# Optimization experiments

Measured on AMD Instinct MI355X. Metric: run time of the kernel, lower is better.

The kernel has to match this reference:

```python
import jax, jax.numpy as jnp
import numpy as np

B, S, D, H = 4, 1024, 768, 12
Dh = D // H
EPS = 1e-5


def _layer_norm(x, g, b):
    mu = jnp.mean(x, axis=-1, keepdims=True)
    var = jnp.var(x, axis=-1, keepdims=True)
    return (x - mu) * jax.lax.rsqrt(var + EPS) * g + b


def _mha(q_in, k_in, v_in, Wq, Wk, Wv, Wo, bias):
    # Wq/Wk/Wv: [H, D, Dh] (per-head projections, batched over heads)
    q = jnp.einsum('bsd,hdk->bhsk', q_in, Wq)
    k = jnp.einsum('btd,hdk->bhtk', k_in, Wk)
    v = jnp.einsum('btd,hdk->bhtk', v_in, Wv)
    w = jnp.einsum('bhsk,bhtk->bhst', q, k) * (Dh ** -0.5)
    a = jax.nn.softmax(w + bias, axis=-1)  # bias: 0 / -inf additive mask
    o = jnp.einsum('bhst,bhtk->bhsk', a, v)
    o = o.transpose(0, 2, 1, 3).reshape(q_in.shape[0], q_in.shape[1], H * Dh)  # concat heads
    return o @ Wo


def setup_inputs():
    key = jax.random.key(0)
    ks = jax.random.split(key, 16)
    s = 0.02
    inp = {
        'key_enc': jax.random.normal(ks[0], (B, S, D), jnp.float32),
        'value_enc': jax.random.normal(ks[1], (B, S, D), jnp.float32),
        'x': jax.random.normal(ks[2], (B, S, D), jnp.float32),
        'src_mask': jnp.ones((B, S), jnp.int32),
        'tgt_mask': jnp.ones((B, S), jnp.int32),
        'Wq_m': jax.random.normal(ks[3], (H, D, Dh), jnp.float32) * s,
        'Wk_m': jax.random.normal(ks[4], (H, D, Dh), jnp.float32) * s,
        'Wv_m': jax.random.normal(ks[5], (H, D, Dh), jnp.float32) * s,
        'Wo_m': jax.random.normal(ks[6], (D, D), jnp.float32) * s,
        'Wq_c': jax.random.normal(ks[7], (H, D, Dh), jnp.float32) * s,
        'Wk_c': jax.random.normal(ks[8], (H, D, Dh), jnp.float32) * s,
        'Wv_c': jax.random.normal(ks[9], (H, D, Dh), jnp.float32) * s,
        'Wo_c': jax.random.normal(ks[10], (D, D), jnp.float32) * s,
        'ln1_g': jnp.ones((D,), jnp.float32), 'ln1_b': jnp.zeros((D,), jnp.float32),
        'ln2_g': jnp.ones((D,), jnp.float32), 'ln2_b': jnp.zeros((D,), jnp.float32),
        'ln3_g': jnp.ones((D,), jnp.float32), 'ln3_b': jnp.zeros((D,), jnp.float32),
        'W1': jax.random.normal(ks[11], (D, 4 * D), jnp.float32) * s,
        'b1': jnp.zeros((4 * D,), jnp.float32),
        'W2': jax.random.normal(ks[12], (4 * D, D), jnp.float32) * s,
        'b2': jnp.zeros((D,), jnp.float32),
    }
    return inp


def reference(key_enc, value_enc, x, src_mask, tgt_mask,
              Wq_m, Wk_m, Wv_m, Wo_m, Wq_c, Wk_c, Wv_c, Wo_c,
              ln1_g, ln1_b, ln2_g, ln2_b, ln3_g, ln3_b, W1, b1, W2, b2):
    neg_inf = jnp.float32(-jnp.inf)
    causal = jnp.tril(jnp.ones((S, S), bool))
    # masked self-attn: causal AND target padding mask (mask broadcasts over query rows)
    allow_m = causal[None, None, :, :] & (tgt_mask[:, None, None, :] != 0)
    bias_m = jnp.where(allow_m, jnp.float32(0.0), neg_inf)
    h = _layer_norm(x + _mha(x, x, x, Wq_m, Wk_m, Wv_m, Wo_m, bias_m), ln1_g, ln1_b)
    # cross-attn: keys from `key_enc`, values from `value_enc`, queries from decoder stream
    allow_c = (src_mask[:, None, None, :] != 0)
    bias_c = jnp.where(allow_c, jnp.float32(0.0), neg_inf)
    h = _layer_norm(h + _mha(h, key_enc, value_enc, Wq_c, Wk_c, Wv_c, Wo_c, bias_c), ln2_g, ln2_b)
    # MLP with exact (erf) GELU, as torch nn.GELU default
    mlp = jax.nn.gelu(h @ W1 + b1, approximate=False) @ W2 + b2
    return _layer_norm(h + mlp, ln3_g, ln3_b)
```

## Files before the change

kernel.cpp:

```cpp
#include <hip/hip_runtime.h>
#include <math.h>

#define BB 4
#define SS 1024
#define DD 768
#define HH 12
#define DHD 64
#define MROWS 4096
#define FF 3072
#define WPC (DD * DD)

typedef unsigned short u16;
typedef float f32x4 __attribute__((ext_vector_type(4)));
typedef __bf16 bf16x8 __attribute__((ext_vector_type(8)));
typedef unsigned short u16x8 __attribute__((ext_vector_type(8)));
typedef unsigned short u16x4 __attribute__((ext_vector_type(4)));

static __device__ __forceinline__ float bf2f(u16 u) {
    union { unsigned int i; float f; } c; c.i = ((unsigned int)u) << 16; return c.f;
}
static __device__ __forceinline__ u16 f2bf(float f) {
    return __builtin_bit_cast(u16, static_cast<__bf16>(f));
}
static __device__ __forceinline__ int xcd_swz(int total) {
    const int bid = (int)blockIdx.x;
    return (bid & 7) * (total >> 3) + (bid >> 3);
}

#define LDST 40

static __device__ __forceinline__ void gemm128_core(
    const u16* __restrict__ A, const u16* __restrict__ Bt,
    int K,
    const float* __restrict__ bias, int do_gelu,
    u16* __restrict__ Cbf, int ldcbf, int cboff,
    int row0, int col0, u16* As, u16* Bs)
{
    const int tid  = threadIdx.x;
    const int lane = tid & 63;
    const int w    = tid >> 6;
    const int wm = (w >> 1) * 64;
    const int wn = (w & 1) * 64;

    const int srow = tid >> 1;
    const int skc  = (tid & 1) * 16;

    const u16* Ap = A  + (size_t)(row0 + srow) * K + skc;
    const u16* Bp = Bt + (size_t)(col0 + srow) * K + skc;
    u16* AsW = &As[srow * LDST + skc];
    u16* BsW = &Bs[srow * LDST + skc];

    const int fr = lane & 15;
    const int fk = (lane >> 4) * 8;

    f32x4 acc[4][4] = {};

    u16x8 aa0, aa1, ba0, ba1;
    u16x8 ab0, ab1, bb0, bb1;
    aa0 = *(const u16x8*)(Ap);
    aa1 = *(const u16x8*)(Ap + 8);
    ba0 = *(const u16x8*)(Bp);
    ba1 = *(const u16x8*)(Bp + 8);
    ab0 = *(const u16x8*)(Ap + 32);
    ab1 = *(const u16x8*)(Ap + 40);
    bb0 = *(const u16x8*)(Bp + 32);
    bb1 = *(const u16x8*)(Bp + 40);

    for (int k0 = 0; k0 < K; k0 += 64) {
        if (k0) __syncthreads();
        *(u16x8*)(AsW)     = aa0;
        *(u16x8*)(AsW + 8) = aa1;
        *(u16x8*)(BsW)     = ba0;
        *(u16x8*)(BsW + 8) = ba1;
        __syncthreads();
        if (k0 + 64 < K) {
            aa0 = *(const u16x8*)(Ap + k0 + 64);
            aa1 = *(const u16x8*)(Ap + k0 + 72);
            ba0 = *(const u16x8*)(Bp + k0 + 64);
            ba1 = *(const u16x8*)(Bp + k0 + 72);
        }
        {
            bf16x8 af[4], bfv[4];
#pragma unroll
            for (int mi = 0; mi < 4; ++mi)
                af[mi] = __builtin_bit_cast(bf16x8,
                    *(const u16x8*)(&As[(wm + 16 * mi + fr) * LDST + fk]));
#pragma unroll
            for (int ni = 0; ni < 4; ++ni)
                bfv[ni] = __builtin_bit_cast(bf16x8,
                    *(const u16x8*)(&Bs[(wn + 16 * ni + fr) * LDST + fk]));
#pragma unroll
            for (int mi = 0; mi < 4; ++mi)
#pragma unroll
                for (int ni = 0; ni < 4; ++ni)
                    acc[mi][ni] = __builtin_amdgcn_mfma_f32_16x16x32_bf16(
                        af[mi], bfv[ni], acc[mi][ni], 0, 0, 0);
        }

        __syncthreads();
        *(u16x8*)(AsW)     = ab0;
        *(u16x8*)(AsW + 8) = ab1;
        *(u16x8*)(BsW)     = bb0;
        *(u16x8*)(BsW + 8) = bb1;
        __syncthreads();
        if (k0 + 96 < K) {
            ab0 = *(const u16x8*)(Ap + k0 + 96);
            ab1 = *(const u16x8*)(Ap + k0 + 104);
            bb0 = *(const u16x8*)(Bp + k0 + 96);
            bb1 = *(const u16x8*)(Bp + k0 + 104);
        }
        {
            bf16x8 af[4], bfv[4];
#pragma unroll
            for (int mi = 0; mi < 4; ++mi)
                af[mi] = __builtin_bit_cast(bf16x8,
                    *(const u16x8*)(&As[(wm + 16 * mi + fr) * LDST + fk]));
#pragma unroll
            for (int ni = 0; ni < 4; ++ni)
                bfv[ni] = __builtin_bit_cast(bf16x8,
                    *(const u16x8*)(&Bs[(wn + 16 * ni + fr) * LDST + fk]));
#pragma unroll
            for (int mi = 0; mi < 4; ++mi)
#pragma unroll
                for (int ni = 0; ni < 4; ++ni)
                    acc[mi][ni] = __builtin_amdgcn_mfma_f32_16x16x32_bf16(
                        af[mi], bfv[ni], acc[mi][ni], 0, 0, 0);
        }
    }

    const int orow0 = row0 + wm + (lane >> 4) * 4;
    const int ocol0 = col0 + wn + fr;
#pragma unroll
    for (int mi = 0; mi < 4; ++mi) {
#pragma unroll
        for (int ni = 0; ni < 4; ++ni) {
            const int col = ocol0 + ni * 16;
            const float bv = bias ? bias[col] : 0.0f;
#pragma unroll
            for (int r = 0; r < 4; ++r) {
                const int row = orow0 + mi * 16 + r;
                float v = acc[mi][ni][r] + bv;
                if (do_gelu) v = 0.5f * v * (1.0f + erff(v * 0.70710678118654752f));
                Cbf[(size_t)row * ldcbf + cboff + col] = f2bf(v);
            }
        }
    }
}

__global__ __launch_bounds__(256) void gemm128_mlp1(
    const u16* __restrict__ A, const u16* __restrict__ Bt,
    const float* __restrict__ bias, u16* __restrict__ Cbf)
{
    __shared__ u16 As[128 * LDST];
    __shared__ u16 Bs[128 * LDST];
    const int lid = xcd_swz(24 * 32);
    gemm128_core(A, Bt, DD, bias, 1, Cbf, FF, 0,
                 (lid / 24) * 128, (lid % 24) * 128, As, Bs);
}

__global__ __launch_bounds__(256) void gemm128_proj(
    const u16* __restrict__ BFx, const u16* __restrict__ BFK,
    const u16* __restrict__ BFV, const u16* __restrict__ Wm6,
    u16* __restrict__ QKV, u16* __restrict__ KVc)
{
    __shared__ u16 As[128 * LDST];
    __shared__ u16 Bs[128 * LDST];
    const int fid = xcd_swz(960);
    const u16* A; const u16* B; u16* C; int ldc, coff, row0, col0;
    if (fid < 576) {
        A = BFx; B = Wm6; C = QKV; ldc = 3 * DD; coff = 0;
        row0 = (fid / 18) * 128; col0 = (fid % 18) * 128;
    } else if (fid < 768) {
        const int l = fid - 576;
        A = BFK; B = Wm6 + 4 * WPC; C = KVc; ldc = 2 * DD; coff = 0;
        row0 = (l / 6) * 128; col0 = (l % 6) * 128;
    } else {
        const int l = fid - 768;
        A = BFV; B = Wm6 + 5 * WPC; C = KVc; ldc = 2 * DD; coff = DD;
        row0 = (l / 6) * 128; col0 = (l % 6) * 128;
    }
    gemm128_core(A, B, DD, nullptr, 0, C, ldc, coff, row0, col0, As, Bs);
}

static __device__ __forceinline__ void gemm64_core(
    const u16* __restrict__ A, const u16* __restrict__ Bt,
    int N, int Kstride, int Klen,
    const float* __restrict__ bias,
    const float* __restrict__ residf, const u16* __restrict__ residb,
    u16* __restrict__ Cbf, int ldcbf, int cboff,
    int row0, int col0, u16* As, u16* Bs)
{
    const int tid  = threadIdx.x;
    const int lane = tid & 63;
    const int w    = tid >> 6;
    const int wm = (w >> 1) * 32;
    const int wn = (w & 1) * 64;

    const int arow = tid >> 2;
    const int akc  = (tid & 3) * 8;
    const int brow = tid >> 1;
    const int bkc  = (tid & 1) * 16;

    const u16* Ap = A  + (size_t)(row0 + arow) * Kstride + akc;
    const u16* Bp = Bt + (size_t)(col0 + brow) * Kstride + bkc;
    u16* AsW = &As[arow * LDST + akc];
    u16* BsW = &Bs[brow * LDST + bkc];

    const int fr = lane & 15;
    const int fk = (lane >> 4) * 8;

    f32x4 acc[2][4] = {};

    u16x8 a0, b00, b01, a1, b10, b11;
    a0  = *(const u16x8*)(Ap);
    b00 = *(const u16x8*)(Bp);
    b01 = *(const u16x8*)(Bp + 8);
    a1  = *(const u16x8*)(Ap + 32);
    b10 = *(const u16x8*)(Bp + 32);
    b11 = *(const u16x8*)(Bp + 40);

    for (int k0 = 0; k0 < Klen; k0 += 64) {
        if (k0) __syncthreads();
        *(u16x8*)AsW       = a0;
        *(u16x8*)BsW       = b00;
        *(u16x8*)(BsW + 8) = b01;
        __syncthreads();
        if (k0 + 64 < Klen) {
            a0  = *(const u16x8*)(Ap + k0 + 64);
            b00 = *(const u16x8*)(Bp + k0 + 64);
            b01 = *(const u16x8*)(Bp + k0 + 72);
        }
        {
            bf16x8 af[2], bfv[4];
#pragma unroll
            for (int mi = 0; mi < 2; ++mi)
                af[mi] = __builtin_bit_cast(bf16x8,
                    *(const u16x8*)(&As[(wm + 16 * mi + fr) * LDST + fk]));
#pragma unroll
            for (int ni = 0; ni < 4; ++ni)
                bfv[ni] = __builtin_bit_cast(bf16x8,
                    *(const u16x8*)(&Bs[(wn + 16 * ni + fr) * LDST + fk]));
#pragma unroll
            for (int mi = 0; mi < 2; ++mi)
#pragma unroll
                for (int ni = 0; ni < 4; ++ni)
                    acc[mi][ni] = __builtin_amdgcn_mfma_f32_16x16x32_bf16(
                        af[mi], bfv[ni], acc[mi][ni], 0, 0, 0);
        }

        __syncthreads();
        *(u16x8*)AsW       = a1;
        *(u16x8*)BsW       = b10;
        *(u16x8*)(BsW + 8) = b11;
        __syncthreads();
        if (k0 + 96 < Klen) {
            a1  = *(const u16x8*)(Ap + k0 + 96);
            b10 = *(const u16x8*)(Bp + k0 + 96);
            b11 = *(const u16x8*)(Bp + k0 + 104);
        }
        {
            bf16x8 af[2], bfv[4];
#pragma unroll
            for (int mi = 0; mi < 2; ++mi)
                af[mi] = __builtin_bit_cast(bf16x8,
                    *(const u16x8*)(&As[(wm + 16 * mi + fr) * LDST + fk]));
#pragma unroll
            for (int ni = 0; ni < 4; ++ni)
                bfv[ni] = __builtin_bit_cast(bf16x8,
                    *(const u16x8*)(&Bs[(wn + 16 * ni + fr) * LDST + fk]));
#pragma unroll
            for (int mi = 0; mi < 2; ++mi)
#pragma unroll
                for (int ni = 0; ni < 4; ++ni)
                    acc[mi][ni] = __builtin_amdgcn_mfma_f32_16x16x32_bf16(
                        af[mi], bfv[ni], acc[mi][ni], 0, 0, 0);
        }
    }

    const int orow0 = row0 + wm + (lane >> 4) * 4;
    const int ocol0 = col0 + wn + fr;
#pragma unroll
    for (int mi = 0; mi < 2; ++mi) {
#pragma unroll
        for (int ni = 0; ni < 4; ++ni) {
            const int col = ocol0 + ni * 16;
            const float bv = bias ? bias[col] : 0.0f;
#pragma unroll
            for (int r = 0; r < 4; ++r) {
                const int row = orow0 + mi * 16 + r;
                float v = acc[mi][ni][r] + bv;
                if (residf) v += residf[(size_t)row * N + col];
                if (residb) v += bf2f(residb[(size_t)row * N + col]);
                Cbf[(size_t)row * ldcbf + cboff + col] = f2bf(v);
            }
        }
    }
}

__global__ __launch_bounds__(256) void gemm64(
    const u16* __restrict__ A, const u16* __restrict__ Bt, int K,
    const float* __restrict__ residf, const u16* __restrict__ residb,
    u16* __restrict__ Cbf, int ldcbf)
{
    __shared__ u16 As[64 * LDST];
    __shared__ u16 Bs[128 * LDST];
    const int lid = xcd_swz(6 * 64);
    gemm64_core(A, Bt, DD, K, K, nullptr, residf, residb, Cbf, ldcbf, 0,
                (lid / 6) * 64, (lid % 6) * 128, As, Bs);
}

__global__ __launch_bounds__(256) void gemm64_sk(
    const u16* __restrict__ A, const u16* __restrict__ Bt,
    u16* __restrict__ Cpair)
{
    __shared__ u16 As[64 * LDST];
    __shared__ u16 Bs[128 * LDST];
    const int lid = xcd_swz(6 * 64 * 2);
    const int x = lid % 6;
    const int rem = lid / 6;
    const int y = rem % 64;
    const int z = rem / 64;
    const int koff = z * (FF / 2);
    gemm64_core(A + koff, Bt + koff, DD, FF, FF / 2,
                nullptr, nullptr, nullptr,
                Cpair + (size_t)z * MROWS * DD, DD, 0,
                y * 64, x * 128, As, Bs);
}

static __device__ __forceinline__ void tcvt_body(
    const float* __restrict__ in, u16* __restrict__ out,
    int K, int N, int bx, int by)
{
    __shared__ float t[32][33];
    const int n0 = bx * 32, k0 = by * 32;
    const int tx = threadIdx.x & 31, ty = threadIdx.x >> 5;
#pragma unroll
    for (int j = 0; j < 4; ++j)
        t[ty + j * 8][tx] = in[(size_t)(k0 + ty + j * 8) * N + n0 + tx];
    __syncthreads();
#pragma unroll
    for (int j = 0; j < 4; ++j)
        out[(size_t)(n0 + ty + j * 8) * K + k0 + tx] = f2bf(t[tx][ty + j * 8]);
}

__global__ __launch_bounds__(256) void prep_all(
    const float* __restrict__ x, const float* __restrict__ key_enc,
    const float* __restrict__ value_enc,
    u16* __restrict__ BFx, u16* __restrict__ BFK, u16* __restrict__ BFV,
    const float* __restrict__ wq_m, const float* __restrict__ wk_m,
    const float* __restrict__ wv_m, const float* __restrict__ wq_c,
    const float* __restrict__ wk_c, const float* __restrict__ wv_c,
    u16* __restrict__ Wm6,
    const float* __restrict__ wom, const float* __restrict__ woc,
    const float* __restrict__ w1, const float* __restrict__ w2,
    u16* __restrict__ womt, u16* __restrict__ woct,
    u16* __restrict__ w1t, u16* __restrict__ w2t)
{
    const int fid = (int)blockIdx.x;
    const int tid = threadIdx.x;
    if (fid < 9216) {
        const int z = fid / 3072;
        const float* s = (z == 0) ? x : (z == 1) ? key_enc : value_enc;
        u16* d = (z == 0) ? BFx : (z == 1) ? BFK : BFV;
        const int i = (fid % 3072) * 256 + tid;
        float4 v = ((const float4*)s)[i];
        ushort4 o;
        o.x = f2bf(v.x); o.y = f2bf(v.y); o.z = f2bf(v.z); o.w = f2bf(v.w);
        ((ushort4*)d)[i] = o;
    } else if (fid < 12672) {
        const int l = fid - 9216;
        const int z = l / 48;
        const int r = l % 48;
        const int wi = z / 12, head = z % 12;
        const float* wsel = (wi == 0) ? wq_m : (wi == 1) ? wk_m :
                            (wi == 2) ? wv_m : (wi == 3) ? wq_c :
                            (wi == 4) ? wk_c : wv_c;
        const float* ib = wsel + (size_t)head * DD * DHD;
        u16* ob = Wm6 + (size_t)wi * WPC + (size_t)head * DHD * DD;
        __shared__ float t[32][33];
        const int n0 = (r % 2) * 32, k0 = (r / 2) * 32;
        const int tx = tid & 31, ty = tid >> 5;
#pragma unroll
        for (int j = 0; j < 4; ++j)
            t[ty + j * 8][tx] = ib[(size_t)(k0 + ty + j * 8) * DHD + n0 + tx];
        __syncthreads();
#pragma unroll
        for (int j = 0; j < 4; ++j)
            ob[(size_t)(n0 + ty + j * 8) * DD + k0 + tx] = f2bf(t[tx][ty + j * 8]);
    } else {
        const int l = fid - 12672;
        if (l < 576) {
            tcvt_body(wom, womt, DD, DD, l % 24, l / 24);
        } else if (l < 1152) {
            const int m = l - 576;
            tcvt_body(woc, woct, DD, DD, m % 24, m / 24);
        } else if (l < 3456) {
            const int m = l - 1152;
            tcvt_body(w1, w1t, DD, FF, m % 96, m / 96);
        } else {
            const int m = l - 3456;
            tcvt_body(w2, w2t, FF, DD, m % 24, m / 24);
        }
    }
}

#define KAST 72
#define PAST 136
#define CSC 0.18033688011112042f
__global__ __launch_bounds__(256) void attn_mfma_kernel(
    const u16* __restrict__ Q, int ldq,
    const u16* __restrict__ K, const u16* __restrict__ V, int ldkv,
    const int* __restrict__ kmask, u16* __restrict__ O, int causal)
{
    const int lid = xcd_swz(16 * BB * HH);
    const int qtl = lid % 16;
    const int bh  = lid / 16;
    const int qt = causal ? (15 - qtl) : qtl;
    const int b  = bh / HH;
    const int h  = bh % HH;
    const int tid  = threadIdx.x;
    const int lane = tid & 63;
    const int w    = tid >> 6;
    const int lr = lane & 15;
    const int lg = lane >> 4;

    __shared__ u16 Ks[128 * KAST];
    __shared__ u16 Ps[64 * PAST];
    __shared__ u16 Vt[64 * PAST];

    const int row0 = qt * 64;
    const int q0w  = row0 + w * 16;

    bf16x8 qf[2];
    {
        const u16* qp = Q + (size_t)(b * SS + q0w + lr) * ldq + h * DHD + lg * 8;
        qf[0] = __builtin_bit_cast(bf16x8, *(const u16x8*)(qp));
        qf[1] = __builtin_bit_cast(bf16x8, *(const u16x8*)(qp + 32));
    }

    const int sr  = tid >> 1;
    const int scb = (tid & 1) * 32;
    const int vk  = tid >> 1;
    const int vdb = (tid & 1) * 32;
    const int k6  = vk & 63;
    const int vcol = ((vk >> 6) << 6) | ((k6 & 15) << 2) | (k6 >> 4);

    f32x4 acc[4] = {};
    float lsum[4] = {0.0f, 0.0f, 0.0f, 0.0f};

    const int nkt = causal ? ((qt + 2) >> 1) : 8;

    u16x8 kr0, kr1, kr2, kr3, vr0, vr1, vr2, vr3;
    {
        const u16* kp = K + (size_t)(b * SS + sr) * ldkv + h * DHD + scb;
        kr0 = *(const u16x8*)(kp);
        kr1 = *(const u16x8*)(kp + 8);
        kr2 = *(const u16x8*)(kp + 16);
        kr3 = *(const u16x8*)(kp + 24);
        const u16* vp = V + (size_t)(b * SS + vk) * ldkv + h * DHD + vdb;
        vr0 = *(const u16x8*)(vp);
        vr1 = *(const u16x8*)(vp + 8);
        vr2 = *(const u16x8*)(vp + 16);
        vr3 = *(const u16x8*)(vp + 24);
    }

    for (int kt = 0; kt < nkt; ++kt) {
        const int kcol0 = kt * 128;
        if (kt) __syncthreads();

        *(u16x8*)(&Ks[sr * KAST + scb])      = kr0;
        *(u16x8*)(&Ks[sr * KAST + scb + 8])  = kr1;
        *(u16x8*)(&Ks[sr * KAST + scb + 16]) = kr2;
        *(u16x8*)(&Ks[sr * KAST + scb + 24]) = kr3;
#pragma unroll
        for (int j = 0; j < 8; ++j) Vt[(vdb + j) * PAST + vcol]      = vr0[j];
#pragma unroll
        for (int j = 0; j < 8; ++j) Vt[(vdb + 8 + j) * PAST + vcol]  = vr1[j];
#pragma unroll
        for (int j = 0; j < 8; ++j) Vt[(vdb + 16 + j) * PAST + vcol] = vr2[j];
#pragma unroll
        for (int j = 0; j < 8; ++j) Vt[(vdb + 24 + j) * PAST + vcol] = vr3[j];
        __syncthreads();

        if (kt + 1 < nkt) {
            const int kn = kcol0 + 128;
            const u16* kp = K + (size_t)(b * SS + kn + sr) * ldkv + h * DHD + scb;
            kr0 = *(const u16x8*)(kp);
            kr1 = *(const u16x8*)(kp + 8);
            kr2 = *(const u16x8*)(kp + 16);
            kr3 = *(const u16x8*)(kp + 24);
            const u16* vp = V + (size_t)(b * SS + kn + vk) * ldkv + h * DHD + vdb;
            vr0 = *(const u16x8*)(vp);
            vr1 = *(const u16x8*)(vp + 8);
            vr2 = *(const u16x8*)(vp + 16);
            vr3 = *(const u16x8*)(vp + 24);
        }

        f32x4 s[8] = {};
#pragma unroll
        for (int fi = 0; fi < 8; ++fi) {
            bf16x8 kf0 = __builtin_bit_cast(bf16x8, *(const u16x8*)(&Ks[(fi * 16 + lr) * KAST + lg * 8]));
            bf16x8 kf1 = __builtin_bit_cast(bf16x8, *(const u16x8*)(&Ks[(fi * 16 + lr) * KAST + 32 + lg * 8]));
            s[fi] = __builtin_amdgcn_mfma_f32_16x16x32_bf16(qf[0], kf0, s[fi], 0, 0, 0);
            s[fi] = __builtin_amdgcn_mfma_f32_16x16x32_bf16(qf[1], kf1, s[fi], 0, 0, 0);
        }

        float biasf[8];
#pragma unroll
        for (int fi = 0; fi < 8; ++fi)
            biasf[fi] = kmask[b * SS + kcol0 + fi * 16 + lr] ? 0.0f : -INFINITY;
        const bool diag = (causal != 0) && (kt == nkt - 1);

#pragma unroll
        for (int r = 0; r < 4; ++r) {
            const int qrow = q0w + lg * 4 + r;
            const int prow = (w * 16 + lg * 4 + r) * PAST;
            u16x4 pk0, pk1;
            float rs = 0.0f;
#pragma unroll
            for (int fi = 0; fi < 8; ++fi) {
                float v = fmaf(s[fi][r], CSC, biasf[fi]);
                if (diag) {
                    const int key = kcol0 + fi * 16 + lr;
                    v = (key <= qrow) ? v : -INFINITY;
                }
                const float pv = exp2f(v);
                if (fi < 4) pk0[fi] = f2bf(pv); else pk1[fi - 4] = f2bf(pv);
                rs += pv;
            }
            lsum[r] += rs;
            *(u16x4*)(&Ps[prow + lr * 4])      = pk0;
            *(u16x4*)(&Ps[prow + 64 + lr * 4]) = pk1;
        }

#pragma unroll
        for (int kk = 0; kk < 4; ++kk) {
            bf16x8 pf = __builtin_bit_cast(bf16x8, *(const u16x8*)(&Ps[(w * 16 + lr) * PAST + kk * 32 + lg * 8]));
#pragma unroll
            for (int di = 0; di < 4; ++di) {
                bf16x8 vf = __builtin_bit_cast(bf16x8, *(const u16x8*)(&Vt[(di * 16 + lr) * PAST + kk * 32 + lg * 8]));
                acc[di] = __builtin_amdgcn_mfma_f32_16x16x32_bf16(pf, vf, acc[di], 0, 0, 0);
            }
        }
    }

#pragma unroll
    for (int r = 0; r < 4; ++r) {
        float l = lsum[r];
        l += __shfl_xor(l, 1);
        l += __shfl_xor(l, 2);
        l += __shfl_xor(l, 4);
        l += __shfl_xor(l, 8);
        const float inv = (l > 0.0f) ? (1.0f / l) : 0.0f;
        const size_t orow = (size_t)(b * SS + q0w + lg * 4 + r) * DD + h * DHD;
#pragma unroll
        for (int di = 0; di < 4; ++di)
            O[orow + di * 16 + lr] = f2bf(acc[di][r] * inv);
    }
}

__global__ __launch_bounds__(256) void ln_bf_kernel(
    const u16* __restrict__ X, const float* __restrict__ gma,
    const float* __restrict__ bta, u16* __restrict__ Ybf)
{
    const int row = blockIdx.x;
    const int tid = threadIdx.x;
    const u16* x = X + (size_t)row * DD;

    const float v0 = bf2f(x[tid]);
    const float v1 = bf2f(x[tid + 256]);
    const float v2 = bf2f(x[tid + 512]);

    __shared__ float sd[256];
    sd[tid] = v0 + v1 + v2;
    __syncthreads();
    for (int off = 128; off > 0; off >>= 1) {
        if (tid < off) sd[tid] += sd[tid + off];
        __syncthreads();
    }
    const float mean = sd[0] * (1.0f / 768.0f);
    __syncthreads();

    const float q0 = v0 - mean, q1 = v1 - mean, q2 = v2 - mean;
    sd[tid] = q0 * q0 + q1 * q1 + q2 * q2;
    __syncthreads();
    for (int off = 128; off > 0; off >>= 1) {
        if (tid < off) sd[tid] += sd[tid + off];
        __syncthreads();
    }
    const float var = sd[0] * (1.0f / 768.0f);
    const float inv = rsqrtf(var + 1e-5f);

    u16* yb = Ybf + (size_t)row * DD;
    yb[tid]       = f2bf(q0 * inv * gma[tid]       + bta[tid]);
    yb[tid + 256] = f2bf(q1 * inv * gma[tid + 256] + bta[tid + 256]);
    yb[tid + 512] = f2bf(q2 * inv * gma[tid + 512] + bta[tid + 512]);
}

__global__ __launch_bounds__(256) void ln_red_kernel(
    const u16* __restrict__ P0, const u16* __restrict__ P1,
    const float* __restrict__ bias, const u16* __restrict__ resid,
    const float* __restrict__ gma, const float* __restrict__ bta,
    float* __restrict__ Y)
{
    const int row = blockIdx.x;
    const int tid = threadIdx.x;
    const size_t base = (size_t)row * DD;

    float v[3];
#pragma unroll
    for (int j = 0; j < 3; ++j) {
        const int i = tid + j * 256;
        v[j] = bf2f(P0[base + i]) + bf2f(P1[base + i]) + bias[i] + bf2f(resid[base + i]);
    }

    __shared__ float sd[256];
    sd[tid] = v[0] + v[1] + v[2];
    __syncthreads();
    for (int off = 128; off > 0; off >>= 1) {
        if (tid < off) sd[tid] += sd[tid + off];
        __syncthreads();
    }
    const float mean = sd[0] * (1.0f / 768.0f);
    __syncthreads();

    float q[3];
#pragma unroll
    for (int j = 0; j < 3; ++j) q[j] = v[j] - mean;
    sd[tid] = q[0] * q[0] + q[1] * q[1] + q[2] * q[2];
    __syncthreads();
    for (int off = 128; off > 0; off >>= 1) {
        if (tid < off) sd[tid] += sd[tid + off];
        __syncthreads();
    }
    const float var = sd[0] * (1.0f / 768.0f);
    const float inv = rsqrtf(var + 1e-5f);

    float* y = Y + base;
#pragma unroll
    for (int j = 0; j < 3; ++j) {
        const int i = tid + j * 256;
        y[i] = q[j] * inv * gma[i] + bta[i];
    }
}

extern "C" void kernel_launch(void* const* d_in, const int* in_sizes, int n_in,
                              void* d_out, int out_size, void* d_ws, size_t ws_size,
                              hipStream_t stream)
{
    (void)in_sizes; (void)n_in; (void)out_size; (void)ws_size;

    const float* key_enc   = (const float*)d_in[0];
    const float* value_enc = (const float*)d_in[1];
    const float* x         = (const float*)d_in[2];
    const int*   src_mask  = (const int*)d_in[3];
    const int*   tgt_mask  = (const int*)d_in[4];
    const float* Wq_m = (const float*)d_in[5];
    const float* Wk_m = (const float*)d_in[6];
    const float* Wv_m = (const float*)d_in[7];
    const float* Wo_m = (const float*)d_in[8];
    const float* Wq_c = (const float*)d_in[9];
    const float* Wk_c = (const float*)d_in[10];
    const float* Wv_c = (const float*)d_in[11];
    const float* Wo_c = (const float*)d_in[12];
    const float* ln1_g = (const float*)d_in[13];
    const float* ln1_b = (const float*)d_in[14];
    const float* ln2_g = (const float*)d_in[15];
    const float* ln2_b = (const float*)d_in[16];
    const float* ln3_g = (const float*)d_in[17];
    const float* ln3_b = (const float*)d_in[18];
    const float* W1 = (const float*)d_in[19];
    const float* b1 = (const float*)d_in[20];
    const float* W2 = (const float*)d_in[21];
    const float* b2 = (const float*)d_in[22];

    float* out = (float*)d_out;

    const size_t ACT = (size_t)MROWS * DD;
    char* p = (char*)d_ws;
    u16* QKV  = (u16*)p;   p += 3 * ACT * 2;
    u16* BFx  = (u16*)p;   p += ACT * 2;
    u16* BFK  = (u16*)p;   p += ACT * 2;
    u16* BFV  = (u16*)p;   p += ACT * 2;
    u16* BF1a = (u16*)p;   p += ACT * 2;
    u16* BF1h = (u16*)p;   p += ACT * 2;
    u16* T2bf = (u16*)p;   p += ACT * 2;
    u16* SKKV = (u16*)p;   p += 2 * ACT * 2;
    u16* Wm6  = (u16*)p;   p += 6 * (size_t)WPC * 2;
    u16* Wom_t = (u16*)p;  p += (size_t)WPC * 2;
    u16* Woc_t = (u16*)p;  p += (size_t)WPC * 2;
    u16* W1t  = (u16*)p;   p += (size_t)DD * FF * 2;
    u16* W2t  = (u16*)p;   p += (size_t)DD * FF * 2;
    u16* MID  = QKV;
    u16* KVc  = SKKV;
    u16* SK0  = SKKV;
    u16* SK1  = SKKV + ACT;

    const dim3 blk(256);

    prep_all<<<dim3(18432), blk, 0, stream>>>(
        x, key_enc, value_enc, BFx, BFK, BFV,
        Wq_m, Wk_m, Wv_m, Wq_c, Wk_c, Wv_c, Wm6,
        Wo_m, Wo_c, W1, W2, Wom_t, Woc_t, W1t, W2t);

    const dim3 gProj(960);
    const dim3 gSkinny(384);
    const dim3 gM1(768);
    const dim3 gM2(768);
    const dim3 gAttn(768);

    gemm128_proj<<<gProj, blk, 0, stream>>>(BFx, BFK, BFV, Wm6, QKV, KVc);

    attn_mfma_kernel<<<gAttn, blk, 0, stream>>>(
        QKV, 3 * DD, QKV + DD, QKV + 2 * DD, 3 * DD, tgt_mask, BF1a, 1);
    gemm64<<<gSkinny, blk, 0, stream>>>(BF1a, Wom_t, DD,
                                        x, nullptr, T2bf, DD);
    ln_bf_kernel<<<MROWS, blk, 0, stream>>>(T2bf, ln1_g, ln1_b, BF1h);

    gemm64<<<gSkinny, blk, 0, stream>>>(BF1h, Wm6 + 3 * WPC, DD,
                                        nullptr, nullptr, QKV, 3 * DD);
    attn_mfma_kernel<<<gAttn, blk, 0, stream>>>(
        QKV, 3 * DD, KVc, KVc + DD, 2 * DD, src_mask, BF1a, 0);
    gemm64<<<gSkinny, blk, 0, stream>>>(BF1a, Woc_t, DD,
                                        nullptr, BF1h, T2bf, DD);
    ln_bf_kernel<<<MROWS, blk, 0, stream>>>(T2bf, ln2_g, ln2_b, BF1h);

    gemm128_mlp1<<<gM1, blk, 0, stream>>>(BF1h, W1t, b1, MID);
    gemm64_sk<<<gM2, blk, 0, stream>>>(MID, W2t, SKKV);
    ln_red_kernel<<<MROWS, blk, 0, stream>>>(SK0, SK1, b2, BF1h,
                                             ln3_g, ln3_b, out);
}
```

Baseline: 291.0 us.

## Split long causal attention tiles across two blocks with a merge kernel

Causal self-attention is moved into its own kernel, where query tiles 8-15, which have the most key tiles, are split into two halves of the key range handled by separate blocks. Each half writes unnormalized bf16 partial outputs and row sums to a workspace, and a new merge kernel combines them. The goal is to balance load and shorten the critical path of the heavy blocks. The cost is an extra launch, extra global traffic, and bf16 rounding of the partial accumulators. Merging without a max is valid only because the softmax here skips max subtraction.

```diff
diff --git a/kernel.cpp b/kernel.cpp
--- a/kernel.cpp
+++ b/kernel.cpp
@@ -9,6 +9,7 @@
 #define MROWS 4096
 #define FF 3072
 #define WPC (DD * DD)
+#define NSPLITROWS 24576
 
 typedef unsigned short u16;
 typedef float f32x4 __attribute__((ext_vector_type(4)));
@@ -407,15 +408,15 @@
 #define KAST 72
 #define PAST 136
 #define CSC 0.18033688011112042f
-__global__ __launch_bounds__(256) void attn_mfma_kernel(
+
+__global__ __launch_bounds__(256) void attn_cross_kernel(
     const u16* __restrict__ Q, int ldq,
     const u16* __restrict__ K, const u16* __restrict__ V, int ldkv,
-    const int* __restrict__ kmask, u16* __restrict__ O, int causal)
+    const int* __restrict__ kmask, u16* __restrict__ O)
 {
     const int lid = xcd_swz(16 * BB * HH);
-    const int qtl = lid % 16;
-    const int bh  = lid / 16;
-    const int qt = causal ? (15 - qtl) : qtl;
+    const int qt = lid % 16;
+    const int bh = lid / 16;
     const int b  = bh / HH;
     const int h  = bh % HH;
     const int tid  = threadIdx.x;
@@ -428,8 +429,7 @@
     __shared__ u16 Ps[64 * PAST];
     __shared__ u16 Vt[64 * PAST];
 
-    const int row0 = qt * 64;
-    const int q0w  = row0 + w * 16;
+    const int q0w = qt * 64 + w * 16;
 
     bf16x8 qf[2];
     {
@@ -447,8 +447,6 @@
 
     f32x4 acc[4] = {};
     float lsum[4] = {0.0f, 0.0f, 0.0f, 0.0f};
-
-    const int nkt = causal ? ((qt + 2) >> 1) : 8;
 
     u16x8 kr0, kr1, kr2, kr3, vr0, vr1, vr2, vr3;
     {
@@ -464,7 +462,7 @@
         vr3 = *(const u16x8*)(vp + 24);
     }
 
-    for (int kt = 0; kt < nkt; ++kt) {
+    for (int kt = 0; kt < 8; ++kt) {
         const int kcol0 = kt * 128;
         if (kt) __syncthreads();
 
@@ -482,7 +480,7 @@
         for (int j = 0; j < 8; ++j) Vt[(vdb + 24 + j) * PAST + vcol] = vr3[j];
         __syncthreads();
 
-        if (kt + 1 < nkt) {
+        if (kt + 1 < 8) {
             const int kn = kcol0 + 128;
             const u16* kp = K + (size_t)(b * SS + kn + sr) * ldkv + h * DHD + scb;
             kr0 = *(const u16x8*)(kp);
@@ -509,7 +507,168 @@
 #pragma unroll
         for (int fi = 0; fi < 8; ++fi)
             biasf[fi] = kmask[b * SS + kcol0 + fi * 16 + lr] ? 0.0f : -INFINITY;
-        const bool diag = (causal != 0) && (kt == nkt - 1);
+
+#pragma unroll
+        for (int r = 0; r < 4; ++r) {
+            const int prow = (w * 16 + lg * 4 + r) * PAST;
+            u16x4 pk0, pk1;
+            float rs = 0.0f;
+#pragma unroll
+            for (int fi = 0; fi < 8; ++fi) {
+                const float v = fmaf(s[fi][r], CSC, biasf[fi]);
+                const float pv = exp2f(v);
+                if (fi < 4) pk0[fi] = f2bf(pv); else pk1[fi - 4] = f2bf(pv);
+                rs += pv;
+            }
+            lsum[r] += rs;
+            *(u16x4*)(&Ps[prow + lr * 4])      = pk0;
+            *(u16x4*)(&Ps[prow + 64 + lr * 4]) = pk1;
+        }
+
+#pragma unroll
+        for (int kk = 0; kk < 4; ++kk) {
+            bf16x8 pf = __builtin_bit_cast(bf16x8, *(const u16x8*)(&Ps[(w * 16 + lr) * PAST + kk * 32 + lg * 8]));
+#pragma unroll
+            for (int di = 0; di < 4; ++di) {
+                bf16x8 vf = __builtin_bit_cast(bf16x8, *(const u16x8*)(&Vt[(di * 16 + lr) * PAST + kk * 32 + lg * 8]));
+                acc[di] = __builtin_amdgcn_mfma_f32_16x16x32_bf16(pf, vf, acc[di], 0, 0, 0);
+            }
+        }
+    }
+
+#pragma unroll
+    for (int r = 0; r < 4; ++r) {
+        float l = lsum[r];
+        l += __shfl_xor(l, 1);
+        l += __shfl_xor(l, 2);
+        l += __shfl_xor(l, 4);
+        l += __shfl_xor(l, 8);
+        const float inv = (l > 0.0f) ? (1.0f / l) : 0.0f;
+        const size_t orow = (size_t)(b * SS + q0w + lg * 4 + r) * DD + h * DHD;
+#pragma unroll
+        for (int di = 0; di < 4; ++di)
+            O[orow + di * 16 + lr] = f2bf(acc[di][r] * inv);
+    }
+}
+
+__global__ __launch_bounds__(256) void attn_self_kernel(
+    const u16* __restrict__ Q, int ldq,
+    const u16* __restrict__ K, const u16* __restrict__ V, int ldkv,
+    const int* __restrict__ kmask, u16* __restrict__ O,
+    u16* __restrict__ ACCP, float* __restrict__ LP)
+{
+    const int lid = xcd_swz(1152);
+    int bh, qt, sp, split;
+    if (lid < 768) {
+        bh = lid / 16;
+        const int t = lid % 16;
+        qt = 8 + (t >> 1);
+        sp = t & 1;
+        split = 1;
+    } else {
+        const int l = lid - 768;
+        bh = l / 8;
+        qt = l % 8;
+        sp = 0;
+        split = 0;
+    }
+    const int b  = bh / HH;
+    const int h  = bh % HH;
+    const int tid  = threadIdx.x;
+    const int lane = tid & 63;
+    const int w    = tid >> 6;
+    const int lr = lane & 15;
+    const int lg = lane >> 4;
+
+    __shared__ u16 Ks[128 * KAST];
+    __shared__ u16 Ps[64 * PAST];
+    __shared__ u16 Vt[64 * PAST];
+
+    const int q0w = qt * 64 + w * 16;
+
+    bf16x8 qf[2];
+    {
+        const u16* qp = Q + (size_t)(b * SS + q0w + lr) * ldq + h * DHD + lg * 8;
+        qf[0] = __builtin_bit_cast(bf16x8, *(const u16x8*)(qp));
+        qf[1] = __builtin_bit_cast(bf16x8, *(const u16x8*)(qp + 32));
+    }
+
+    const int sr  = tid >> 1;
+    const int scb = (tid & 1) * 32;
+    const int vk  = tid >> 1;
+    const int vdb = (tid & 1) * 32;
+    const int k6  = vk & 63;
+    const int vcol = ((vk >> 6) << 6) | ((k6 & 15) << 2) | (k6 >> 4);
+
+    f32x4 acc[4] = {};
+    float lsum[4] = {0.0f, 0.0f, 0.0f, 0.0f};
+
+    const int nktF = (qt + 2) >> 1;
+    const int h2   = (nktF + 1) >> 1;
+    const int ktBeg = split ? (sp ? h2 : 0) : 0;
+    const int ktEnd = split ? (sp ? nktF : h2) : nktF;
+
+    u16x8 kr0, kr1, kr2, kr3, vr0, vr1, vr2, vr3;
+    {
+        const int kn = ktBeg * 128;
+        const u16* kp = K + (size_t)(b * SS + kn + sr) * ldkv + h * DHD + scb;
+        kr0 = *(const u16x8*)(kp);
+        kr1 = *(const u16x8*)(kp + 8);
+        kr2 = *(const u16x8*)(kp + 16);
+        kr3 = *(const u16x8*)(kp + 24);
+        const u16* vp = V + (size_t)(b * SS + kn + vk) * ldkv + h * DHD + vdb;
+        vr0 = *(const u16x8*)(vp);
+        vr1 = *(const u16x8*)(vp + 8);
+        vr2 = *(const u16x8*)(vp + 16);
+        vr3 = *(const u16x8*)(vp + 24);
+    }
+
+    for (int kt = ktBeg; kt < ktEnd; ++kt) {
+        const int kcol0 = kt * 128;
+        if (kt != ktBeg) __syncthreads();
+
+        *(u16x8*)(&Ks[sr * KAST + scb])      = kr0;
+        *(u16x8*)(&Ks[sr * KAST + scb + 8])  = kr1;
+        *(u16x8*)(&Ks[sr * KAST + scb + 16]) = kr2;
+        *(u16x8*)(&Ks[sr * KAST + scb + 24]) = kr3;
+#pragma unroll
+        for (int j = 0; j < 8; ++j) Vt[(vdb + j) * PAST + vcol]      = vr0[j];
+#pragma unroll
+        for (int j = 0; j < 8; ++j) Vt[(vdb + 8 + j) * PAST + vcol]  = vr1[j];
+#pragma unroll
+        for (int j = 0; j < 8; ++j) Vt[(vdb + 16 + j) * PAST + vcol] = vr2[j];
+#pragma unroll
+        for (int j = 0; j < 8; ++j) Vt[(vdb + 24 + j) * PAST + vcol] = vr3[j];
+        __syncthreads();
+
+        if (kt + 1 < ktEnd) {
+            const int kn = kcol0 + 128;
+            const u16* kp = K + (size_t)(b * SS + kn + sr) * ldkv + h * DHD + scb;
+            kr0 = *(const u16x8*)(kp);
+            kr1 = *(const u16x8*)(kp + 8);
+            kr2 = *(const u16x8*)(kp + 16);
+            kr3 = *(const u16x8*)(kp + 24);
+            const u16* vp = V + (size_t)(b * SS + kn + vk) * ldkv + h * DHD + vdb;
+            vr0 = *(const u16x8*)(vp);
+            vr1 = *(const u16x8*)(vp + 8);
+            vr2 = *(const u16x8*)(vp + 16);
+            vr3 = *(const u16x8*)(vp + 24);
+        }
+
+        f32x4 s[8] = {};
+#pragma unroll
+        for (int fi = 0; fi < 8; ++fi) {
+            bf16x8 kf0 = __builtin_bit_cast(bf16x8, *(const u16x8*)(&Ks[(fi * 16 + lr) * KAST + lg * 8]));
+            bf16x8 kf1 = __builtin_bit_cast(bf16x8, *(const u16x8*)(&Ks[(fi * 16 + lr) * KAST + 32 + lg * 8]));
+            s[fi] = __builtin_amdgcn_mfma_f32_16x16x32_bf16(qf[0], kf0, s[fi], 0, 0, 0);
+            s[fi] = __builtin_amdgcn_mfma_f32_16x16x32_bf16(qf[1], kf1, s[fi], 0, 0, 0);
+        }
+
+        float biasf[8];
+#pragma unroll
+        for (int fi = 0; fi < 8; ++fi)
+            biasf[fi] = kmask[b * SS + kcol0 + fi * 16 + lr] ? 0.0f : -INFINITY;
+        const bool diag = (kt == nktF - 1);
 
 #pragma unroll
         for (int r = 0; r < 4; ++r) {
@@ -551,12 +710,47 @@
         l += __shfl_xor(l, 2);
         l += __shfl_xor(l, 4);
         l += __shfl_xor(l, 8);
-        const float inv = (l > 0.0f) ? (1.0f / l) : 0.0f;
-        const size_t orow = (size_t)(b * SS + q0w + lg * 4 + r) * DD + h * DHD;
-#pragma unroll
-        for (int di = 0; di < 4; ++di)
-            O[orow + di * 16 + lr] = f2bf(acc[di][r] * inv);
-    }
+        if (!split) {
+            const float inv = (l > 0.0f) ? (1.0f / l) : 0.0f;
+            const size_t orow = (size_t)(b * SS + q0w + lg * 4 + r) * DD + h * DHD;
+#pragma unroll
+            for (int di = 0; di < 4; ++di)
+                O[orow + di * 16 + lr] = f2bf(acc[di][r] * inv);
+        } else {
+            const int R = bh * 512 + (qt - 8) * 64 + w * 16 + lg * 4 + r;
+            u16* ap = ACCP + ((size_t)sp * NSPLITROWS + R) * 64;
+#pragma unroll
+            for (int di = 0; di < 4; ++di)
+                ap[di * 16 + lr] = f2bf(acc[di][r]);
+            if (lr == 0)
+                LP[sp * NSPLITROWS + R] = l;
+        }
+    }
+}
+
+__global__ __launch_bounds__(256) void attn_merge_kernel(
+    const u16* __restrict__ ACCP, const float* __restrict__ LP,
+    u16* __restrict__ O)
+{
+    const int gid = (int)blockIdx.x * 256 + threadIdx.x;
+    const int R  = gid >> 3;
+    const int d0 = (gid & 7) * 8;
+    const float l0 = LP[R];
+    const float l1 = LP[NSPLITROWS + R];
+    const float den = l0 + l1;
+    const float inv = (den > 0.0f) ? (1.0f / den) : 0.0f;
+    u16x8 a0 = *(const u16x8*)(ACCP + (size_t)R * 64 + d0);
+    u16x8 a1 = *(const u16x8*)(ACCP + ((size_t)NSPLITROWS + R) * 64 + d0);
+    u16x8 o;
+#pragma unroll
+    for (int j = 0; j < 8; ++j)
+        o[j] = f2bf((bf2f(a0[j]) + bf2f(a1[j])) * inv);
+    const int bh = R >> 9;
+    const int r  = R & 511;
+    const int b  = bh / HH;
+    const int h  = bh % HH;
+    const size_t orow = (size_t)(b * SS + 512 + r) * DD + h * DHD;
+    *(u16x8*)(O + orow + d0) = o;
 }
 
 __global__ __launch_bounds__(256) void ln_bf_kernel(
@@ -691,10 +885,12 @@
     u16* Woc_t = (u16*)p;  p += (size_t)WPC * 2;
     u16* W1t  = (u16*)p;   p += (size_t)DD * FF * 2;
     u16* W2t  = (u16*)p;   p += (size_t)DD * FF * 2;
+    float* LP = (float*)p; p += 2 * (size_t)NSPLITROWS * 4;
     u16* MID  = QKV;
     u16* KVc  = SKKV;
     u16* SK0  = SKKV;
     u16* SK1  = SKKV + ACT;
+    u16* ACCP = T2bf;
 
     const dim3 blk(256);
 
@@ -703,30 +899,25 @@
         Wq_m, Wk_m, Wv_m, Wq_c, Wk_c, Wv_c, Wm6,
         Wo_m, Wo_c, W1, W2, Wom_t, Woc_t, W1t, W2t);
 
-    const dim3 gProj(960);
-    const dim3 gSkinny(384);
-    const dim3 gM1(768);
-    const dim3 gM2(768);
-    const dim3 gAttn(768);
-
-    gemm128_proj<<<gProj, blk, 0, stream>>>(BFx, BFK, BFV, Wm6, QKV, KVc);
-
-    attn_mfma_kernel<<<gAttn, blk, 0, stream>>>(
-        QKV, 3 * DD, QKV + DD, QKV + 2 * DD, 3 * DD, tgt_mask, BF1a, 1);
-    gemm64<<<gSkinny, blk, 0, stream>>>(BF1a, Wom_t, DD,
-                                        x, nullptr, T2bf, DD);
+    gemm128_proj<<<dim3(960), blk, 0, stream>>>(BFx, BFK, BFV, Wm6, QKV, KVc);
+
+    attn_self_kernel<<<dim3(1152), blk, 0, stream>>>(
+        QKV, 3 * DD, QKV + DD, QKV + 2 * DD, 3 * DD, tgt_mask, BF1a, ACCP, LP);
+    attn_merge_kernel<<<dim3(768), blk, 0, stream>>>(ACCP, LP, BF1a);
+    gemm64<<<dim3(384), blk, 0, stream>>>(BF1a, Wom_t, DD,
+                                          x, nullptr, T2bf, DD);
     ln_bf_kernel<<<MROWS, blk, 0, stream>>>(T2bf, ln1_g, ln1_b, BF1h);
 
-    gemm64<<<gSkinny, blk, 0, stream>>>(BF1h, Wm6 + 3 * WPC, DD,
-                                        nullptr, nullptr, QKV, 3 * DD);
-    attn_mfma_kernel<<<gAttn, blk, 0, stream>>>(
-        QKV, 3 * DD, KVc, KVc + DD, 2 * DD, src_mask, BF1a, 0);
-    gemm64<<<gSkinny, blk, 0, stream>>>(BF1a, Woc_t, DD,
-                                        nullptr, BF1h, T2bf, DD);
+    gemm64<<<dim3(384), blk, 0, stream>>>(BF1h, Wm6 + 3 * WPC, DD,
+                                          nullptr, nullptr, QKV, 3 * DD);
+    attn_cross_kernel<<<dim3(768), blk, 0, stream>>>(
+        QKV, 3 * DD, KVc, KVc + DD, 2 * DD, src_mask, BF1a);
+    gemm64<<<dim3(384), blk, 0, stream>>>(BF1a, Woc_t, DD,
+                                          nullptr, BF1h, T2bf, DD);
     ln_bf_kernel<<<MROWS, blk, 0, stream>>>(T2bf, ln2_g, ln2_b, BF1h);
 
-    gemm128_mlp1<<<gM1, blk, 0, stream>>>(BF1h, W1t, b1, MID);
-    gemm64_sk<<<gM2, blk, 0, stream>>>(MID, W2t, SKKV);
+    gemm128_mlp1<<<dim3(768), blk, 0, stream>>>(BF1h, W1t, b1, MID);
+    gemm64_sk<<<dim3(768), blk, 0, stream>>>(MID, W2t, SKKV);
     ln_red_kernel<<<MROWS, blk, 0, stream>>>(SK0, SK1, b2, BF1h,
                                              ln3_g, ln3_b, out);
 }
```

Result: no change. 291.4 us (+0.1%).
